# Kernel tuning notes

Hardware: AMD Instinct MI355X
Metric: run time of the kernel (lower is better)

## Reference

```python
import jax, jax.numpy as jnp
import numpy as np

B, N, M, F = 32, 1024, 1024, 64


def setup_inputs() -> dict:
    key = jax.random.key(0)
    kx, ky = jax.random.split(key)
    x = jax.random.normal(kx, (B, N, F), dtype=jnp.float32)
    y = jax.random.normal(ky, (B, M, F), dtype=jnp.float32)
    return {"x": x, "y": y}


def _cdist(x, y):
    # torch.cdist(x, y, p=2): [N, M] euclidean distance matrix via GEMM form
    sq = (jnp.sum(x * x, axis=-1)[:, None]
          + jnp.sum(y * y, axis=-1)[None, :]
          - 2.0 * (x @ y.T))
    return jnp.sqrt(jnp.maximum(sq, 0.0))


def _dtw_single(x, y):
    # Classic DTW DP: D[i,j] = cost[i,j] + min(D[i-1,j], D[i,j-1], D[i-1,j-1])
    # with D[0,0]=0 and inf boundaries. The inner (j) recurrence
    #   cur[j] = cost[j] + min(m[j], cur[j-1]),  m[j] = min(prev[j], prev[j-1])
    # is a min-plus prefix scan solvable in closed form:
    #   cur[j] = C[j] + cummin_j(cost[j] + m[j] - C[j]),  C = cumsum(cost)
    # which vectorizes each row (wavefront-equivalent, no O(M) python loop).
    dist = _cdist(x, y)  # [N, M]
    m = dist.shape[1]
    init = jnp.concatenate([jnp.zeros((1,), dist.dtype),
                            jnp.full((m,), jnp.inf, dist.dtype)])  # D[0, :]

    def row_step(prev, cost_row):
        mins = jnp.minimum(prev[1:], prev[:-1])          # min(up, diag), [M]
        C = jnp.cumsum(cost_row)                         # [M]
        cur = C + jax.lax.cummin(cost_row + mins - C)    # [M]
        prev_new = jnp.concatenate(
            [jnp.full((1,), jnp.inf, dist.dtype), cur])  # D[i, 0] = inf
        return prev_new, None

    last, _ = jax.lax.scan(row_step, init, dist)
    return last[-1]  # D[N, M]


def reference(x, y):
    # batched forward, distances per pair: [B]
    return jax.vmap(_dtw_single)(x, y)
```

## Files before the change

### kernel.cpp

```cpp
#include <hip/hip_runtime.h>
#include <math.h>

#define BB 32
#define NN 1024
#define MM 1024
#define FF 64
#define INF_ 1e30f

typedef float f32x4 __attribute__((ext_vector_type(4)));

__global__ __launch_bounds__(256) void norms_kernel(const float* __restrict__ x,
                                                    const float* __restrict__ y,
                                                    float* __restrict__ xn,
                                                    float* __restrict__ yn) {
    int gw = (blockIdx.x * 256 + threadIdx.x) >> 6;
    int lane = threadIdx.x & 63;
    int total = BB * NN + BB * MM;
    if (gw >= total) return;
    const float* src; float* dst; int row;
    if (gw < BB * NN) { src = x; dst = xn; row = gw; }
    else             { src = y; dst = yn; row = gw - BB * NN; }
    float v = src[(size_t)row * FF + lane];
    float s = v * v;
    #pragma unroll
    for (int d = 32; d > 0; d >>= 1) s += __shfl_xor(s, d, 64);
    if (lane == 0) dst[row] = s;
}

__global__ __launch_bounds__(256) void cost_kernel(const float* __restrict__ x,
                                                   const float* __restrict__ y,
                                                   const float* __restrict__ xn,
                                                   const float* __restrict__ yn,
                                                   float* __restrict__ cost) {
    __shared__ float Xs[FF][68];
    __shared__ float Ys[FF][68];
    const int b    = blockIdx.z;
    const int row0 = blockIdx.y * 64;
    const int col0 = blockIdx.x * 64;
    const int tid  = threadIdx.x;
    const float* xb = x + (size_t)b * NN * FF;
    const float* yb = y + (size_t)b * MM * FF;

    #pragma unroll
    for (int cc = 0; cc < 4; ++cc) {
        int s  = tid + cc * 256;
        int r  = s >> 4;
        int kq = s & 15;
        float4 vx = *(const float4*)(xb + (size_t)(row0 + r) * FF + kq * 4);
        float4 vy = *(const float4*)(yb + (size_t)(col0 + r) * FF + kq * 4);
        Xs[kq*4+0][r] = vx.x; Xs[kq*4+1][r] = vx.y; Xs[kq*4+2][r] = vx.z; Xs[kq*4+3][r] = vx.w;
        Ys[kq*4+0][r] = vy.x; Ys[kq*4+1][r] = vy.y; Ys[kq*4+2][r] = vy.z; Ys[kq*4+3][r] = vy.w;
    }
    __syncthreads();

    const int tx = tid & 15, ty = tid >> 4;
    float acc[4][4] = {};
    #pragma unroll 16
    for (int k = 0; k < FF; ++k) {
        float4 a  = *(const float4*)&Xs[k][ty * 4];
        float4 bb = *(const float4*)&Ys[k][tx * 4];
        float av[4] = {a.x, a.y, a.z, a.w};
        float bv[4] = {bb.x, bb.y, bb.z, bb.w};
        #pragma unroll
        for (int r = 0; r < 4; ++r)
            #pragma unroll
            for (int c = 0; c < 4; ++c)
                acc[r][c] += av[r] * bv[c];
    }

    float* cD = cost + (size_t)b * NN * MM;
    #pragma unroll
    for (int r = 0; r < 4; ++r) {
        int row = row0 + ty * 4 + r;
        float xnv = xn[b * NN + row];
        #pragma unroll
        for (int c = 0; c < 4; ++c) {
            int col = col0 + tx * 4 + c;
            float v = xnv + yn[b * MM + col] - 2.0f * acc[r][c];
            v = sqrtf(fmaxf(v, 0.0f));
            cD[(size_t)((row + col) & 1023) * MM + row] = v;
        }
    }
}

__device__ __forceinline__ float dpp_wave_shr1(float v, float oldv) {
    int t = __builtin_amdgcn_update_dpp(__float_as_int(oldv), __float_as_int(v),
                                        0x138, 0xf, 0xf, false);
    return __int_as_float(t);
}

struct RowBuf { f32x4 q0, q1, q2, q3; };

__device__ __forceinline__ void issue_row(RowBuf& R, const float* rowbase,
                                          unsigned voff) {
    asm volatile(
        "global_load_dwordx4 %0, %4, %5\n\t"
        "global_load_dwordx4 %1, %4, %5 offset:16\n\t"
        "global_load_dwordx4 %2, %4, %5 offset:32\n\t"
        "global_load_dwordx4 %3, %4, %5 offset:48"
        : "=v"(R.q0), "=v"(R.q1), "=v"(R.q2), "=v"(R.q3)
        : "v"(voff), "s"(rowbase));
}

__global__ __launch_bounds__(64)
__attribute__((amdgpu_waves_per_eu(1, 1)))
void dtw_diag_kernel(const float* __restrict__ cost, float* __restrict__ out) {
    const int b    = blockIdx.x;
    const int lane = threadIdx.x;
    const float* cbD = cost + (size_t)b * NN * MM;
    const unsigned voff = (unsigned)lane * 64u;

    RowBuf R0, R1, R2, R3, R4, R5, R6, R7;
    issue_row(R0, cbD + 0 * (size_t)MM, voff);
    issue_row(R1, cbD + 1 * (size_t)MM, voff);
    issue_row(R2, cbD + 2 * (size_t)MM, voff);
    issue_row(R3, cbD + 3 * (size_t)MM, voff);
    issue_row(R4, cbD + 4 * (size_t)MM, voff);
    issue_row(R5, cbD + 5 * (size_t)MM, voff);
    issue_row(R6, cbD + 6 * (size_t)MM, voff);
    issue_row(R7, cbD + 7 * (size_t)MM, voff);

    float A[16], B[16];
    #pragma unroll
    for (int j = 0; j < 16; ++j) { A[j] = INF_; B[j] = INF_; }
    float bnd = 0.0f;

    #define DIAG_STEP(Rk, PV, P2, NR)                                          \
    {                                                                          \
        asm volatile("s_waitcnt vmcnt(28)" ::: "memory");                      \
        __builtin_amdgcn_sched_barrier(0);                                     \
        float cc[16] = {Rk.q0[0], Rk.q0[1], Rk.q0[2], Rk.q0[3],                \
                        Rk.q1[0], Rk.q1[1], Rk.q1[2], Rk.q1[3],                \
                        Rk.q2[0], Rk.q2[1], Rk.q2[2], Rk.q2[3],                \
                        Rk.q3[0], Rk.q3[1], Rk.q3[2], Rk.q3[3]};               \
        float pvm1 = dpp_wave_shr1(PV[15], INF_);                              \
        float p2m1 = dpp_wave_shr1(P2[15], bnd);                               \
        _Pragma("unroll")                                                      \
        for (int r = 0; r < 16; ++r) {                                         \
            float pv_r = PV[r], p2_r = P2[r];                                  \
            P2[r] = cc[r] + fminf(fminf(pv_r, pvm1), p2m1);                    \
            pvm1 = pv_r; p2m1 = p2_r;                                          \
        }                                                                      \
        __builtin_amdgcn_sched_barrier(0);                                     \
        issue_row(Rk, cbD + (size_t)(NR) * MM, voff);                          \
    }

    DIAG_STEP(R0, A, B, 8)   bnd = INF_;
    DIAG_STEP(R1, B, A, 9)
    DIAG_STEP(R2, A, B, 10)
    DIAG_STEP(R3, B, A, 11)
    DIAG_STEP(R4, A, B, 12)
    DIAG_STEP(R5, B, A, 13)
    DIAG_STEP(R6, A, B, 14)
    DIAG_STEP(R7, B, A, 15)

    for (int d0 = 8; d0 < 2040; d0 += 8) {
        DIAG_STEP(R0, A, B, ((d0 +  8) & 1023))
        DIAG_STEP(R1, B, A, ((d0 +  9) & 1023))
        DIAG_STEP(R2, A, B, ((d0 + 10) & 1023))
        DIAG_STEP(R3, B, A, ((d0 + 11) & 1023))
        DIAG_STEP(R4, A, B, ((d0 + 12) & 1023))
        DIAG_STEP(R5, B, A, ((d0 + 13) & 1023))
        DIAG_STEP(R6, A, B, ((d0 + 14) & 1023))
        DIAG_STEP(R7, B, A, ((d0 + 15) & 1023))
    }

    DIAG_STEP(R0, A, B, 0)
    DIAG_STEP(R1, B, A, 1)
    DIAG_STEP(R2, A, B, 2)
    DIAG_STEP(R3, B, A, 3)
    DIAG_STEP(R4, A, B, 4)
    DIAG_STEP(R5, B, A, 5)
    DIAG_STEP(R6, A, B, 6)
    #undef DIAG_STEP

    if (lane == 63) out[b] = B[15];
}

__global__ __launch_bounds__(1024) void dtw_fused_kernel(const float* __restrict__ x,
                                                         const float* __restrict__ y,
                                                         float* __restrict__ out) {
    const int b    = blockIdx.x;
    const int tid  = threadIdx.x;
    const int lane = tid & 63;
    const int wid  = tid >> 6;
    __shared__ float P[MM];
    __shared__ float xrow[FF];
    __shared__ float part_sum[16];
    __shared__ float part_min[16];

    float yr[FF];
    const float* yrow = y + ((size_t)b * MM + tid) * FF;
    #pragma unroll
    for (int q = 0; q < FF / 4; ++q) {
        float4 v = ((const float4*)yrow)[q];
        yr[q*4+0] = v.x; yr[q*4+1] = v.y; yr[q*4+2] = v.z; yr[q*4+3] = v.w;
    }

    P[tid] = INF_;
    __syncthreads();

    const float* xb = x + (size_t)b * NN * FF;
    float result = 0.0f;

    for (int i = 0; i < NN; ++i) {
        if (tid < FF) xrow[tid] = xb[(size_t)i * FF + tid];
        float up   = P[tid];
        float diag = (tid == 0) ? (i == 0 ? 0.0f : INF_) : P[tid - 1];
        float m    = fminf(up, diag);
        __syncthreads();

        float ss = 0.0f;
        #pragma unroll 16
        for (int k = 0; k < FF; ++k) {
            float d = xrow[k] - yr[k];
            ss += d * d;
        }
        float c = sqrtf(ss);

        float s = c;
        #pragma unroll
        for (int d = 1; d < 64; d <<= 1) {
            float t = __shfl_up(s, d, 64);
            if (lane >= d) s += t;
        }
        if (lane == 63) part_sum[wid] = s;
        __syncthreads();
        if (tid < 16) {
            float p = part_sum[tid];
            #pragma unroll
            for (int d = 1; d < 16; d <<= 1) {
                float t = __shfl_up(p, d, 64);
                if (tid >= d) p += t;
            }
            part_sum[tid] = p;
        }
        __syncthreads();
        float C = s + (wid > 0 ? part_sum[wid - 1] : 0.0f);

        float z = c + m - C;
        float w = z;
        #pragma unroll
        for (int d = 1; d < 64; d <<= 1) {
            float t = __shfl_up(w, d, 64);
            if (lane >= d) w = fminf(w, t);
        }
        if (lane == 63) part_min[wid] = w;
        __syncthreads();
        if (tid < 16) {
            float p = part_min[tid];
            #pragma unroll
            for (int d = 1; d < 16; d <<= 1) {
                float t = __shfl_up(p, d, 64);
                if (tid >= d) p = fminf(p, t);
            }
            part_min[tid] = p;
        }
        __syncthreads();
        float wm  = (wid > 0) ? fminf(w, part_min[wid - 1]) : w;
        float cur = C + wm;

        P[tid] = cur;
        __syncthreads();
        if (i == NN - 1 && tid == MM - 1) result = cur;
    }
    if (tid == MM - 1) out[b] = result;
}

extern "C" void kernel_launch(void* const* d_in, const int* in_sizes, int n_in,
                              void* d_out, int out_size, void* d_ws, size_t ws_size,
                              hipStream_t stream) {
    const float* x = (const float*)d_in[0];
    const float* y = (const float*)d_in[1];
    float* out = (float*)d_out;

    size_t need = (size_t)BB * NN * MM * sizeof(float)
                + (size_t)BB * NN * sizeof(float)
                + (size_t)BB * MM * sizeof(float);

    if (ws_size >= need) {
        float* cost = (float*)d_ws;
        float* xn = cost + (size_t)BB * NN * MM;
        float* yn = xn + (size_t)BB * NN;

        int total_rows = BB * NN + BB * MM;
        int blocks = (total_rows + 3) / 4;
        hipLaunchKernelGGL(norms_kernel, dim3(blocks), dim3(256), 0, stream,
                           x, y, xn, yn);
        hipLaunchKernelGGL(cost_kernel, dim3(MM / 64, NN / 64, BB), dim3(256), 0, stream,
                           x, y, xn, yn, cost);
        hipLaunchKernelGGL(dtw_diag_kernel, dim3(BB), dim3(64), 0, stream, cost, out);
    } else {
        hipLaunchKernelGGL(dtw_fused_kernel, dim3(BB), dim3(1024), 0, stream, x, y, out);
    }
}
```

Before: 263.7 us.

## Stream DTW anti-diagonal cost rows through an LDS ring via global_load_lds

The DTW wavefront kernel no longer holds 8 prefetched rows in VGPRs. It now streams each anti-diagonal cost row straight into a 14-slot LDS ring using global_load_lds, which gives a deeper prefetch. The cost producer permutes the column position within each diagonal row so that the 4 dword LDS writes per lane land where each lane can later read its 16 contiguous values with float4 LDS reads. The aim is to hide global-load latency on the serial diagonal chain and to cut register pressure. The cost is extra LDS read latency on the critical path, plus more fragile vmcnt accounting.

```diff
diff --git a/kernel.cpp b/kernel.cpp
--- a/kernel.cpp
+++ b/kernel.cpp
@@ -6,6 +6,7 @@
 #define MM 1024
 #define FF 64
 #define INF_ 1e30f
+#define RING 14
 
 typedef float f32x4 __attribute__((ext_vector_type(4)));
 
@@ -73,12 +74,13 @@
     for (int r = 0; r < 4; ++r) {
         int row = row0 + ty * 4 + r;
         float xnv = xn[b * NN + row];
+        int pos = ((row >> 2) & 3) * 256 + (row >> 4) * 4 + (row & 3);
         #pragma unroll
         for (int c = 0; c < 4; ++c) {
             int col = col0 + tx * 4 + c;
             float v = xnv + yn[b * MM + col] - 2.0f * acc[r][c];
             v = sqrtf(fmaxf(v, 0.0f));
-            cD[(size_t)((row + col) & 1023) * MM + row] = v;
+            cD[(size_t)((row + col) & 1023) * MM + pos] = v;
         }
     }
 }
@@ -89,90 +91,109 @@
     return __int_as_float(t);
 }
 
-struct RowBuf { f32x4 q0, q1, q2, q3; };
-
-__device__ __forceinline__ void issue_row(RowBuf& R, const float* rowbase,
-                                          unsigned voff) {
-    asm volatile(
-        "global_load_dwordx4 %0, %4, %5\n\t"
-        "global_load_dwordx4 %1, %4, %5 offset:16\n\t"
-        "global_load_dwordx4 %2, %4, %5 offset:32\n\t"
-        "global_load_dwordx4 %3, %4, %5 offset:48"
-        : "=v"(R.q0), "=v"(R.q1), "=v"(R.q2), "=v"(R.q3)
-        : "v"(voff), "s"(rowbase));
-}
-
 __global__ __launch_bounds__(64)
 __attribute__((amdgpu_waves_per_eu(1, 1)))
 void dtw_diag_kernel(const float* __restrict__ cost, float* __restrict__ out) {
+    __shared__ float ring[RING * 1024];
     const int b    = blockIdx.x;
     const int lane = threadIdx.x;
     const float* cbD = cost + (size_t)b * NN * MM;
-    const unsigned voff = (unsigned)lane * 64u;
-
-    RowBuf R0, R1, R2, R3, R4, R5, R6, R7;
-    issue_row(R0, cbD + 0 * (size_t)MM, voff);
-    issue_row(R1, cbD + 1 * (size_t)MM, voff);
-    issue_row(R2, cbD + 2 * (size_t)MM, voff);
-    issue_row(R3, cbD + 3 * (size_t)MM, voff);
-    issue_row(R4, cbD + 4 * (size_t)MM, voff);
-    issue_row(R5, cbD + 5 * (size_t)MM, voff);
-    issue_row(R6, cbD + 6 * (size_t)MM, voff);
-    issue_row(R7, cbD + 7 * (size_t)MM, voff);
-
-    float A[16], B[16];
+
+    #define GLL_ROW(NRROW, SLOT)                                               \
+    {                                                                          \
+        const float* rb_ = cbD + (size_t)(NRROW) * MM;                         \
+        _Pragma("unroll")                                                      \
+        for (int k_ = 0; k_ < 4; ++k_) {                                       \
+            __builtin_amdgcn_global_load_lds(                                  \
+                (const __attribute__((address_space(1))) void*)(rb_ + k_ * 256 + lane * 4), \
+                (__attribute__((address_space(3))) void*)(&ring[(SLOT) * 1024 + k_ * 256]), \
+                16, 0, 0);                                                     \
+        }                                                                      \
+    }
+
+    #pragma unroll
+    for (int rr = 0; rr < RING; ++rr) GLL_ROW(rr, rr)
+
+    float A[16], B[16], C0[16], C1[16];
     #pragma unroll
     for (int j = 0; j < 16; ++j) { A[j] = INF_; B[j] = INF_; }
     float bnd = 0.0f;
 
-    #define DIAG_STEP(Rk, PV, P2, NR)                                          \
+    asm volatile("s_waitcnt vmcnt(52)" ::: "memory");
+    {
+        #pragma unroll
+        for (int k = 0; k < 4; ++k) {
+            float4 n = *(const float4*)&ring[k * 256 + lane * 4];
+            C0[4*k+0] = n.x; C0[4*k+1] = n.y; C0[4*k+2] = n.z; C0[4*k+3] = n.w;
+        }
+    }
+
+    #define DIAG_STEP(SLOT_CUR, SLOT_NXT, PV, P2, CC, CCN, NRROW)              \
     {                                                                          \
-        asm volatile("s_waitcnt vmcnt(28)" ::: "memory");                      \
-        __builtin_amdgcn_sched_barrier(0);                                     \
-        float cc[16] = {Rk.q0[0], Rk.q0[1], Rk.q0[2], Rk.q0[3],                \
-                        Rk.q1[0], Rk.q1[1], Rk.q1[2], Rk.q1[3],                \
-                        Rk.q2[0], Rk.q2[1], Rk.q2[2], Rk.q2[3],                \
-                        Rk.q3[0], Rk.q3[1], Rk.q3[2], Rk.q3[3]};               \
         float pvm1 = dpp_wave_shr1(PV[15], INF_);                              \
         float p2m1 = dpp_wave_shr1(P2[15], bnd);                               \
+        float t[16];                                                           \
         _Pragma("unroll")                                                      \
         for (int r = 0; r < 16; ++r) {                                         \
             float pv_r = PV[r], p2_r = P2[r];                                  \
-            P2[r] = cc[r] + fminf(fminf(pv_r, pvm1), p2m1);                    \
+            t[r] = fminf(fminf(pv_r, pvm1), p2m1);                             \
             pvm1 = pv_r; p2m1 = p2_r;                                          \
         }                                                                      \
-        __builtin_amdgcn_sched_barrier(0);                                     \
-        issue_row(Rk, cbD + (size_t)(NR) * MM, voff);                          \
-    }
-
-    DIAG_STEP(R0, A, B, 8)   bnd = INF_;
-    DIAG_STEP(R1, B, A, 9)
-    DIAG_STEP(R2, A, B, 10)
-    DIAG_STEP(R3, B, A, 11)
-    DIAG_STEP(R4, A, B, 12)
-    DIAG_STEP(R5, B, A, 13)
-    DIAG_STEP(R6, A, B, 14)
-    DIAG_STEP(R7, B, A, 15)
-
-    for (int d0 = 8; d0 < 2040; d0 += 8) {
-        DIAG_STEP(R0, A, B, ((d0 +  8) & 1023))
-        DIAG_STEP(R1, B, A, ((d0 +  9) & 1023))
-        DIAG_STEP(R2, A, B, ((d0 + 10) & 1023))
-        DIAG_STEP(R3, B, A, ((d0 + 11) & 1023))
-        DIAG_STEP(R4, A, B, ((d0 + 12) & 1023))
-        DIAG_STEP(R5, B, A, ((d0 + 13) & 1023))
-        DIAG_STEP(R6, A, B, ((d0 + 14) & 1023))
-        DIAG_STEP(R7, B, A, ((d0 + 15) & 1023))
-    }
-
-    DIAG_STEP(R0, A, B, 0)
-    DIAG_STEP(R1, B, A, 1)
-    DIAG_STEP(R2, A, B, 2)
-    DIAG_STEP(R3, B, A, 3)
-    DIAG_STEP(R4, A, B, 4)
-    DIAG_STEP(R5, B, A, 5)
-    DIAG_STEP(R6, A, B, 6)
+        asm volatile("s_waitcnt vmcnt(48)" ::: "memory");                      \
+        float4 n0 = *(const float4*)&ring[(SLOT_NXT) * 1024 + 0 * 256 + lane * 4]; \
+        float4 n1 = *(const float4*)&ring[(SLOT_NXT) * 1024 + 1 * 256 + lane * 4]; \
+        float4 n2 = *(const float4*)&ring[(SLOT_NXT) * 1024 + 2 * 256 + lane * 4]; \
+        float4 n3 = *(const float4*)&ring[(SLOT_NXT) * 1024 + 3 * 256 + lane * 4]; \
+        _Pragma("unroll")                                                      \
+        for (int r = 0; r < 16; ++r) P2[r] = CC[r] + t[r];                     \
+        GLL_ROW(NRROW, SLOT_CUR)                                               \
+        CCN[0]  = n0.x; CCN[1]  = n0.y; CCN[2]  = n0.z; CCN[3]  = n0.w;        \
+        CCN[4]  = n1.x; CCN[5]  = n1.y; CCN[6]  = n1.z; CCN[7]  = n1.w;        \
+        CCN[8]  = n2.x; CCN[9]  = n2.y; CCN[10] = n2.z; CCN[11] = n2.w;        \
+        CCN[12] = n3.x; CCN[13] = n3.y; CCN[14] = n3.z; CCN[15] = n3.w;        \
+    }
+
+    #define BLOCK14(D0)                                                        \
+        DIAG_STEP(0,  1,  A, B, C0, C1, (((D0) + 14) & 1023))                  \
+        DIAG_STEP(1,  2,  B, A, C1, C0, (((D0) + 15) & 1023))                  \
+        DIAG_STEP(2,  3,  A, B, C0, C1, (((D0) + 16) & 1023))                  \
+        DIAG_STEP(3,  4,  B, A, C1, C0, (((D0) + 17) & 1023))                  \
+        DIAG_STEP(4,  5,  A, B, C0, C1, (((D0) + 18) & 1023))                  \
+        DIAG_STEP(5,  6,  B, A, C1, C0, (((D0) + 19) & 1023))                  \
+        DIAG_STEP(6,  7,  A, B, C0, C1, (((D0) + 20) & 1023))                  \
+        DIAG_STEP(7,  8,  B, A, C1, C0, (((D0) + 21) & 1023))                  \
+        DIAG_STEP(8,  9,  A, B, C0, C1, (((D0) + 22) & 1023))                  \
+        DIAG_STEP(9,  10, B, A, C1, C0, (((D0) + 23) & 1023))                  \
+        DIAG_STEP(10, 11, A, B, C0, C1, (((D0) + 24) & 1023))                  \
+        DIAG_STEP(11, 12, B, A, C1, C0, (((D0) + 25) & 1023))                  \
+        DIAG_STEP(12, 13, A, B, C0, C1, (((D0) + 26) & 1023))                  \
+        DIAG_STEP(13, 0,  B, A, C1, C0, (((D0) + 27) & 1023))
+
+    DIAG_STEP(0,  1,  A, B, C0, C1, 14)   bnd = INF_;
+    DIAG_STEP(1,  2,  B, A, C1, C0, 15)
+    DIAG_STEP(2,  3,  A, B, C0, C1, 16)
+    DIAG_STEP(3,  4,  B, A, C1, C0, 17)
+    DIAG_STEP(4,  5,  A, B, C0, C1, 18)
+    DIAG_STEP(5,  6,  B, A, C1, C0, 19)
+    DIAG_STEP(6,  7,  A, B, C0, C1, 20)
+    DIAG_STEP(7,  8,  B, A, C1, C0, 21)
+    DIAG_STEP(8,  9,  A, B, C0, C1, 22)
+    DIAG_STEP(9,  10, B, A, C1, C0, 23)
+    DIAG_STEP(10, 11, A, B, C0, C1, 24)
+    DIAG_STEP(11, 12, B, A, C1, C0, 25)
+    DIAG_STEP(12, 13, A, B, C0, C1, 26)
+    DIAG_STEP(13, 0,  B, A, C1, C0, 27)
+
+    for (int d0 = 14; d0 < 2044; d0 += 14) {
+        BLOCK14(d0)
+    }
+
+    DIAG_STEP(0, 1, A, B, C0, C1, 10)
+    DIAG_STEP(1, 2, B, A, C1, C0, 11)
+    DIAG_STEP(2, 3, A, B, C0, C1, 12)
     #undef DIAG_STEP
+    #undef BLOCK14
+    #undef GLL_ROW
 
     if (lane == 63) out[b] = B[15];
 }
```

Measured after the change: 730.6 us. 177% more time.

## Fuse norms into cost kernel, add prefetch touches and hoist DTW min before wait

Applied to the files above, without the earlier changes.

Removes the separate norms kernel and computes the squared row norms of the x and y tiles from shared memory inside the cost kernel, which drops one launch and the extra global traffic. In the DTW diagonal kernel it issues dummy single-dword loads eight diagonals ahead to warm the cache. It also computes the min-of-neighbours part of each step before waiting on the cost row load, so that ALU work overlaps memory latency. The trade-offs are more outstanding loads per wave (the vmcnt threshold rises from 28 to 36), redundant norm computation in every tile, and a possible dependence on vmcnt ordering.

```diff
diff --git a/kernel.cpp b/kernel.cpp
--- a/kernel.cpp
+++ b/kernel.cpp
@@ -9,31 +9,13 @@
 
 typedef float f32x4 __attribute__((ext_vector_type(4)));
 
-__global__ __launch_bounds__(256) void norms_kernel(const float* __restrict__ x,
-                                                    const float* __restrict__ y,
-                                                    float* __restrict__ xn,
-                                                    float* __restrict__ yn) {
-    int gw = (blockIdx.x * 256 + threadIdx.x) >> 6;
-    int lane = threadIdx.x & 63;
-    int total = BB * NN + BB * MM;
-    if (gw >= total) return;
-    const float* src; float* dst; int row;
-    if (gw < BB * NN) { src = x; dst = xn; row = gw; }
-    else             { src = y; dst = yn; row = gw - BB * NN; }
-    float v = src[(size_t)row * FF + lane];
-    float s = v * v;
-    #pragma unroll
-    for (int d = 32; d > 0; d >>= 1) s += __shfl_xor(s, d, 64);
-    if (lane == 0) dst[row] = s;
-}
-
 __global__ __launch_bounds__(256) void cost_kernel(const float* __restrict__ x,
                                                    const float* __restrict__ y,
-                                                   const float* __restrict__ xn,
-                                                   const float* __restrict__ yn,
                                                    float* __restrict__ cost) {
     __shared__ float Xs[FF][68];
     __shared__ float Ys[FF][68];
+    __shared__ float xnl[64];
+    __shared__ float ynl[64];
     const int b    = blockIdx.z;
     const int row0 = blockIdx.y * 64;
     const int col0 = blockIdx.x * 64;
@@ -53,6 +35,19 @@
     }
     __syncthreads();
 
+    if (tid < 64) {
+        float s = 0.0f;
+        #pragma unroll 16
+        for (int k = 0; k < FF; ++k) { float v = Xs[k][tid]; s += v * v; }
+        xnl[tid] = s;
+    } else if (tid < 128) {
+        int r = tid - 64;
+        float s = 0.0f;
+        #pragma unroll 16
+        for (int k = 0; k < FF; ++k) { float v = Ys[k][r]; s += v * v; }
+        ynl[r] = s;
+    }
+
     const int tx = tid & 15, ty = tid >> 4;
     float acc[4][4] = {};
     #pragma unroll 16
@@ -67,16 +62,19 @@
             for (int c = 0; c < 4; ++c)
                 acc[r][c] += av[r] * bv[c];
     }
+    __syncthreads();
 
     float* cD = cost + (size_t)b * NN * MM;
     #pragma unroll
     for (int r = 0; r < 4; ++r) {
-        int row = row0 + ty * 4 + r;
-        float xnv = xn[b * NN + row];
+        int rl  = ty * 4 + r;
+        int row = row0 + rl;
+        float xnv = xnl[rl];
         #pragma unroll
         for (int c = 0; c < 4; ++c) {
-            int col = col0 + tx * 4 + c;
-            float v = xnv + yn[b * MM + col] - 2.0f * acc[r][c];
+            int cl  = tx * 4 + c;
+            int col = col0 + cl;
+            float v = xnv + ynl[cl] - 2.0f * acc[r][c];
             v = sqrtf(fmaxf(v, 0.0f));
             cD[(size_t)((row + col) & 1023) * MM + row] = v;
         }
@@ -102,6 +100,12 @@
         : "v"(voff), "s"(rowbase));
 }
 
+__device__ __forceinline__ void touch_row(float& dummy, const float* rowbase,
+                                          unsigned voff) {
+    asm volatile("global_load_dword %0, %1, %2"
+                 : "+v"(dummy) : "v"(voff), "s"(rowbase));
+}
+
 __global__ __launch_bounds__(64)
 __attribute__((amdgpu_waves_per_eu(1, 1)))
 void dtw_diag_kernel(const float* __restrict__ cost, float* __restrict__ out) {
@@ -111,68 +115,75 @@
     const unsigned voff = (unsigned)lane * 64u;
 
     RowBuf R0, R1, R2, R3, R4, R5, R6, R7;
-    issue_row(R0, cbD + 0 * (size_t)MM, voff);
-    issue_row(R1, cbD + 1 * (size_t)MM, voff);
-    issue_row(R2, cbD + 2 * (size_t)MM, voff);
-    issue_row(R3, cbD + 3 * (size_t)MM, voff);
-    issue_row(R4, cbD + 4 * (size_t)MM, voff);
-    issue_row(R5, cbD + 5 * (size_t)MM, voff);
-    issue_row(R6, cbD + 6 * (size_t)MM, voff);
-    issue_row(R7, cbD + 7 * (size_t)MM, voff);
+    float dummy = 0.0f;
+    issue_row(R0, cbD + 0 * (size_t)MM, voff);  touch_row(dummy, cbD +  8 * (size_t)MM, voff);
+    issue_row(R1, cbD + 1 * (size_t)MM, voff);  touch_row(dummy, cbD +  9 * (size_t)MM, voff);
+    issue_row(R2, cbD + 2 * (size_t)MM, voff);  touch_row(dummy, cbD + 10 * (size_t)MM, voff);
+    issue_row(R3, cbD + 3 * (size_t)MM, voff);  touch_row(dummy, cbD + 11 * (size_t)MM, voff);
+    issue_row(R4, cbD + 4 * (size_t)MM, voff);  touch_row(dummy, cbD + 12 * (size_t)MM, voff);
+    issue_row(R5, cbD + 5 * (size_t)MM, voff);  touch_row(dummy, cbD + 13 * (size_t)MM, voff);
+    issue_row(R6, cbD + 6 * (size_t)MM, voff);  touch_row(dummy, cbD + 14 * (size_t)MM, voff);
+    issue_row(R7, cbD + 7 * (size_t)MM, voff);  touch_row(dummy, cbD + 15 * (size_t)MM, voff);
 
     float A[16], B[16];
     #pragma unroll
     for (int j = 0; j < 16; ++j) { A[j] = INF_; B[j] = INF_; }
     float bnd = 0.0f;
 
-    #define DIAG_STEP(Rk, PV, P2, NR)                                          \
+    #define DIAG_STEP(Rk, PV, P2, NR, NT)                                      \
     {                                                                          \
-        asm volatile("s_waitcnt vmcnt(28)" ::: "memory");                      \
+        float pvm1 = dpp_wave_shr1(PV[15], INF_);                              \
+        float p2m1 = dpp_wave_shr1(P2[15], bnd);                               \
+        float t[16];                                                           \
+        _Pragma("unroll")                                                      \
+        for (int r = 0; r < 16; ++r) {                                         \
+            float pv_r = PV[r], p2_r = P2[r];                                  \
+            t[r] = fminf(fminf(pv_r, pvm1), p2m1);                             \
+            pvm1 = pv_r; p2m1 = p2_r;                                          \
+        }                                                                      \
+        asm volatile("s_waitcnt vmcnt(36)" ::: "memory");                      \
         __builtin_amdgcn_sched_barrier(0);                                     \
         float cc[16] = {Rk.q0[0], Rk.q0[1], Rk.q0[2], Rk.q0[3],                \
                         Rk.q1[0], Rk.q1[1], Rk.q1[2], Rk.q1[3],                \
                         Rk.q2[0], Rk.q2[1], Rk.q2[2], Rk.q2[3],                \
                         Rk.q3[0], Rk.q3[1], Rk.q3[2], Rk.q3[3]};               \
-        float pvm1 = dpp_wave_shr1(PV[15], INF_);                              \
-        float p2m1 = dpp_wave_shr1(P2[15], bnd);                               \
         _Pragma("unroll")                                                      \
-        for (int r = 0; r < 16; ++r) {                                         \
-            float pv_r = PV[r], p2_r = P2[r];                                  \
-            P2[r] = cc[r] + fminf(fminf(pv_r, pvm1), p2m1);                    \
-            pvm1 = pv_r; p2m1 = p2_r;                                          \
-        }                                                                      \
+        for (int r = 0; r < 16; ++r) P2[r] = cc[r] + t[r];                     \
         __builtin_amdgcn_sched_barrier(0);                                     \
         issue_row(Rk, cbD + (size_t)(NR) * MM, voff);                          \
-    }
-
-    DIAG_STEP(R0, A, B, 8)   bnd = INF_;
-    DIAG_STEP(R1, B, A, 9)
-    DIAG_STEP(R2, A, B, 10)
-    DIAG_STEP(R3, B, A, 11)
-    DIAG_STEP(R4, A, B, 12)
-    DIAG_STEP(R5, B, A, 13)
-    DIAG_STEP(R6, A, B, 14)
-    DIAG_STEP(R7, B, A, 15)
+        touch_row(dummy, cbD + (size_t)(NT) * MM, voff);                       \
+    }
+
+    DIAG_STEP(R0, A, B, 8,  16)   bnd = INF_;
+    DIAG_STEP(R1, B, A, 9,  17)
+    DIAG_STEP(R2, A, B, 10, 18)
+    DIAG_STEP(R3, B, A, 11, 19)
+    DIAG_STEP(R4, A, B, 12, 20)
+    DIAG_STEP(R5, B, A, 13, 21)
+    DIAG_STEP(R6, A, B, 14, 22)
+    DIAG_STEP(R7, B, A, 15, 23)
 
     for (int d0 = 8; d0 < 2040; d0 += 8) {
-        DIAG_STEP(R0, A, B, ((d0 +  8) & 1023))
-        DIAG_STEP(R1, B, A, ((d0 +  9) & 1023))
-        DIAG_STEP(R2, A, B, ((d0 + 10) & 1023))
-        DIAG_STEP(R3, B, A, ((d0 + 11) & 1023))
-        DIAG_STEP(R4, A, B, ((d0 + 12) & 1023))
-        DIAG_STEP(R5, B, A, ((d0 + 13) & 1023))
-        DIAG_STEP(R6, A, B, ((d0 + 14) & 1023))
-        DIAG_STEP(R7, B, A, ((d0 + 15) & 1023))
-    }
-
-    DIAG_STEP(R0, A, B, 0)
-    DIAG_STEP(R1, B, A, 1)
-    DIAG_STEP(R2, A, B, 2)
-    DIAG_STEP(R3, B, A, 3)
-    DIAG_STEP(R4, A, B, 4)
-    DIAG_STEP(R5, B, A, 5)
-    DIAG_STEP(R6, A, B, 6)
+        DIAG_STEP(R0, A, B, ((d0 +  8) & 1023), ((d0 + 16) & 1023))
+        DIAG_STEP(R1, B, A, ((d0 +  9) & 1023), ((d0 + 17) & 1023))
+        DIAG_STEP(R2, A, B, ((d0 + 10) & 1023), ((d0 + 18) & 1023))
+        DIAG_STEP(R3, B, A, ((d0 + 11) & 1023), ((d0 + 19) & 1023))
+        DIAG_STEP(R4, A, B, ((d0 + 12) & 1023), ((d0 + 20) & 1023))
+        DIAG_STEP(R5, B, A, ((d0 + 13) & 1023), ((d0 + 21) & 1023))
+        DIAG_STEP(R6, A, B, ((d0 + 14) & 1023), ((d0 + 22) & 1023))
+        DIAG_STEP(R7, B, A, ((d0 + 15) & 1023), ((d0 + 23) & 1023))
+    }
+
+    DIAG_STEP(R0, A, B, 0, 16)
+    DIAG_STEP(R1, B, A, 1, 17)
+    DIAG_STEP(R2, A, B, 2, 18)
+    DIAG_STEP(R3, B, A, 3, 19)
+    DIAG_STEP(R4, A, B, 4, 20)
+    DIAG_STEP(R5, B, A, 5, 21)
+    DIAG_STEP(R6, A, B, 6, 22)
     #undef DIAG_STEP
+
+    asm volatile("" :: "v"(dummy));
 
     if (lane == 63) out[b] = B[15];
 }
@@ -274,21 +285,12 @@
     const float* y = (const float*)d_in[1];
     float* out = (float*)d_out;
 
-    size_t need = (size_t)BB * NN * MM * sizeof(float)
-                + (size_t)BB * NN * sizeof(float)
-                + (size_t)BB * MM * sizeof(float);
+    size_t need = (size_t)BB * NN * MM * sizeof(float);
 
     if (ws_size >= need) {
         float* cost = (float*)d_ws;
-        float* xn = cost + (size_t)BB * NN * MM;
-        float* yn = xn + (size_t)BB * NN;
-
-        int total_rows = BB * NN + BB * MM;
-        int blocks = (total_rows + 3) / 4;
-        hipLaunchKernelGGL(norms_kernel, dim3(blocks), dim3(256), 0, stream,
-                           x, y, xn, yn);
         hipLaunchKernelGGL(cost_kernel, dim3(MM / 64, NN / 64, BB), dim3(256), 0, stream,
-                           x, y, xn, yn, cost);
+                           x, y, cost);
         hipLaunchKernelGGL(dtw_diag_kernel, dim3(BB), dim3(64), 0, stream, cost, out);
     } else {
         hipLaunchKernelGGL(dtw_fused_kernel, dim3(BB), dim3(1024), 0, stream, x, y, out);
```

Result: slower. 291.5 us (+10.5%).
